# Kernel tuning notes

Measured on AMD Instinct MI355X. Metric: run time of the kernel, lower is better.

Reference implementation:

```python
import jax, jax.numpy as jnp
import numpy as np

GAMMA = 2.0  # args.gamma
B, C, H, W = 8, 21, 512, 512


def setup_inputs() -> dict:
    key = jax.random.key(0)
    k1, k2 = jax.random.split(key)
    pred = jax.random.normal(k1, (B, C, H, W), dtype=jnp.float32)
    # one-hot target built from random per-pixel class labels
    labels = jax.random.randint(k2, (B, H, W), 0, C)
    target = jax.nn.one_hot(labels, C, dtype=jnp.float32)  # [B,H,W,C]
    target = jnp.transpose(target, (0, 3, 1, 2))  # [B,C,H,W]
    return {"pred": pred, "target": target}


def reference(pred, target) -> jnp.ndarray:
    b, c, h, w = pred.shape
    logits = jax.nn.log_softmax(pred, axis=1)  # [B,C,H,W]
    lo = jnp.transpose(logits, (0, 2, 3, 1)).reshape(-1, c)  # [N,C]
    tg = jnp.transpose(target, (0, 2, 3, 1)).reshape(-1, c)  # [N,C]
    n = lo.shape[0]
    beta = (n - 1.0) / n
    # per-pixel focal term summed over channels: sum_j (1-p_j)^gamma * log p_j * t_j
    row_val = jnp.sum((1.0 - jnp.exp(lo)) ** GAMMA * lo * tg, axis=1)  # [N]
    mask = (tg == 1).astype(lo.dtype)  # [N,C] class membership mask
    n_c = jnp.sum(mask, axis=0)  # [C] pixels per class
    class_sum = jnp.einsum('nc,n->c', mask, row_val)  # [C] masked reductions
    w = (1.0 - beta) / (1.0 - jnp.power(jnp.float32(beta), n_c) + 1e-6)  # [C]
    return -jnp.sum(w * class_sum) / n
```

## Files before the change

### kernel.cpp

```cpp
#include <hip/hip_runtime.h>

#define CCH    21
#define HWSZ   (512*512)
#define HW4    (HWSZ/4)
#define NPIX   (8*HWSZ)
#define BLKT   256
#define NBLK   (NPIX/4/BLKT)
#define CB     3
#define NBATCH (CCH/CB)

#define WAIT_VM6() __builtin_amdgcn_s_waitcnt(0x0F70 | 6)
#define WAIT_VM0() __builtin_amdgcn_s_waitcnt(0x0F70 | 0)

typedef float vfloat4 __attribute__((ext_vector_type(4)));

__device__ __forceinline__ void stage16(const float* g, vfloat4* l) {
    __builtin_amdgcn_global_load_lds(
        (const __attribute__((address_space(1))) unsigned int*)g,
        (__attribute__((address_space(3))) unsigned int*)l, 16, 0, 0);
}

__global__ __launch_bounds__(BLKT) void cb_focal_partial(
    const float* __restrict__ pred, const float* __restrict__ targ,
    float* __restrict__ gsum, float* __restrict__ gcnt)
{
    __shared__ vfloat4 sbuf[2][2*CB][BLKT];
    __shared__ float ls_sum[CCH];
    __shared__ float ls_cnt[CCH];
    if (threadIdx.x < CCH) { ls_sum[threadIdx.x] = 0.f; ls_cnt[threadIdx.x] = 0.f; }
    __syncthreads();

    const int tid = blockIdx.x * BLKT + threadIdx.x;
    const int b   = tid >> 16;
    const int hw4 = tid & (HW4 - 1);
    const float* pp = pred + (size_t)b * CCH * HWSZ + (size_t)hw4 * 4;
    const float* tp = targ + (size_t)b * CCH * HWSZ + (size_t)hw4 * 4;
    const int wv = threadIdx.x & 192;

    float s0 = 0.f, s1 = 0.f, s2 = 0.f, s3 = 0.f;
    float vy0 = 0.f, vy1 = 0.f, vy2 = 0.f, vy3 = 0.f;
    float ey0 = 1.f, ey1 = 1.f, ey2 = 1.f, ey3 = 1.f;
    int   y0 = 0, y1 = 0, y2 = 0, y3 = 0;

    auto issue = [&](int k, int buf) {
        #pragma unroll
        for (int j = 0; j < CB; ++j) {
            const size_t coff = (size_t)(k * CB + j) * HWSZ;
            stage16(pp + coff, &sbuf[buf][2*j    ][wv]);
            stage16(tp + coff, &sbuf[buf][2*j + 1][wv]);
        }
    };

    auto compute = [&](int k) {
        #pragma unroll
        for (int j = 0; j < CB; ++j) {
            const vfloat4 v = sbuf[k & 1][2*j    ][threadIdx.x];
            const vfloat4 t = sbuf[k & 1][2*j + 1][threadIdx.x];
            const int c = k * CB + j;
            const float e0 = __expf(v.x), e1 = __expf(v.y),
                        e2 = __expf(v.z), e3 = __expf(v.w);
            s0 += e0; s1 += e1; s2 += e2; s3 += e3;
            const bool h0 = t.x > 0.5f, h1 = t.y > 0.5f,
                       h2 = t.z > 0.5f, h3 = t.w > 0.5f;
            y0 = h0 ? c : y0;  vy0 = h0 ? v.x : vy0;  ey0 = h0 ? e0 : ey0;
            y1 = h1 ? c : y1;  vy1 = h1 ? v.y : vy1;  ey1 = h1 ? e1 : ey1;
            y2 = h2 ? c : y2;  vy2 = h2 ? v.z : vy2;  ey2 = h2 ? e2 : ey2;
            y3 = h3 ? c : y3;  vy3 = h3 ? v.w : vy3;  ey3 = h3 ? e3 : ey3;
        }
    };

    issue(0, 0);
    #pragma unroll
    for (int k = 0; k < NBATCH - 1; ++k) {
        issue(k + 1, (k + 1) & 1);
        __builtin_amdgcn_sched_barrier(0);
        WAIT_VM6();
        __builtin_amdgcn_sched_barrier(0);
        compute(k);
    }
    __builtin_amdgcn_sched_barrier(0);
    WAIT_VM0();
    __builtin_amdgcn_sched_barrier(0);
    compute(NBATCH - 1);

    {
        const float l0 = vy0 - __logf(s0), p0 = ey0 / s0, o0 = 1.f - p0;
        const float l1 = vy1 - __logf(s1), p1 = ey1 / s1, o1 = 1.f - p1;
        const float l2 = vy2 - __logf(s2), p2 = ey2 / s2, o2 = 1.f - p2;
        const float l3 = vy3 - __logf(s3), p3 = ey3 / s3, o3 = 1.f - p3;
        atomicAdd(&ls_sum[y0], o0 * o0 * l0);  atomicAdd(&ls_cnt[y0], 1.f);
        atomicAdd(&ls_sum[y1], o1 * o1 * l1);  atomicAdd(&ls_cnt[y1], 1.f);
        atomicAdd(&ls_sum[y2], o2 * o2 * l2);  atomicAdd(&ls_cnt[y2], 1.f);
        atomicAdd(&ls_sum[y3], o3 * o3 * l3);  atomicAdd(&ls_cnt[y3], 1.f);
    }
    __syncthreads();
    if (threadIdx.x < CCH) {
        atomicAdd(&gsum[threadIdx.x], ls_sum[threadIdx.x]);
        atomicAdd(&gcnt[threadIdx.x], ls_cnt[threadIdx.x]);
    }
}

__global__ void cb_focal_final(const float* __restrict__ gsum,
                               const float* __restrict__ gcnt,
                               float* __restrict__ out)
{
    const int lane = threadIdx.x;
    double term = 0.0;
    if (lane < CCH) {
        const double n    = (double)NPIX;
        const double beta = (n - 1.0) / n;
        const double w = (1.0 - beta) / (1.0 - pow(beta, (double)gcnt[lane]) + 1e-6);
        term = w * (double)gsum[lane];
    }
    for (int off = 32; off; off >>= 1) term += __shfl_down(term, off, 64);
    if (lane == 0) out[0] = (float)(-term / (double)NPIX);
}

extern "C" void kernel_launch(void* const* d_in, const int* in_sizes, int n_in,
                              void* d_out, int out_size, void* d_ws, size_t ws_size,
                              hipStream_t stream) {
    const float* pred = (const float*)d_in[0];
    const float* targ = (const float*)d_in[1];
    float* out  = (float*)d_out;
    float* gsum = (float*)d_ws;
    float* gcnt = gsum + CCH;

    (void)hipMemsetAsync(gsum, 0, 2 * CCH * sizeof(float), stream);
    cb_focal_partial<<<NBLK, BLKT, 0, stream>>>(pred, targ, gsum, gcnt);
    cb_focal_final<<<1, 64, 0, stream>>>(gsum, gcnt, out);
}
```

Measured before the change: 358.4 us.

## Load pred directly into registers, stage only target via LDS in 7-channel batches

Pred values are now read straight into VGPRs with nontemporal vector loads, and only the target tensor is staged through LDS with global_load_lds. Channels are processed in three batches of seven instead of seven batches of three, with double-buffered register and LDS storage. This halves LDS traffic and shared memory use and puts more bytes in flight per wave. In exchange it raises register pressure (two sets of seven vfloat4) and relies on a hand-computed vmcnt wait value being correct.

```diff
diff --git a/kernel.cpp b/kernel.cpp
--- a/kernel.cpp
+++ b/kernel.cpp
@@ -6,11 +6,10 @@
 #define NPIX   (8*HWSZ)
 #define BLKT   256
 #define NBLK   (NPIX/4/BLKT)
-#define CB     3
-#define NBATCH (CCH/CB)
+#define CB     7
+#define NB     3
 
-#define WAIT_VM6() __builtin_amdgcn_s_waitcnt(0x0F70 | 6)
-#define WAIT_VM0() __builtin_amdgcn_s_waitcnt(0x0F70 | 0)
+#define WAIT_VM(n) __builtin_amdgcn_s_waitcnt(0x0F70 | (n))
 
 typedef float vfloat4 __attribute__((ext_vector_type(4)));
 
@@ -24,7 +23,7 @@
     const float* __restrict__ pred, const float* __restrict__ targ,
     float* __restrict__ gsum, float* __restrict__ gcnt)
 {
-    __shared__ vfloat4 sbuf[2][2*CB][BLKT];
+    __shared__ vfloat4 tbuf[2][CB][BLKT];
     __shared__ float ls_sum[CCH];
     __shared__ float ls_cnt[CCH];
     if (threadIdx.x < CCH) { ls_sum[threadIdx.x] = 0.f; ls_cnt[threadIdx.x] = 0.f; }
@@ -42,46 +41,51 @@
     float ey0 = 1.f, ey1 = 1.f, ey2 = 1.f, ey3 = 1.f;
     int   y0 = 0, y1 = 0, y2 = 0, y3 = 0;
 
-    auto issue = [&](int k, int buf) {
+    vfloat4 v[2][CB];
+
+    #pragma unroll
+    for (int j = 0; j < CB; ++j)
+        stage16(tp + (size_t)j * HWSZ, &tbuf[0][j][wv]);
+    #pragma unroll
+    for (int j = 0; j < CB; ++j)
+        v[0][j] = __builtin_nontemporal_load((const vfloat4*)(pp + (size_t)j * HWSZ));
+    __builtin_amdgcn_sched_barrier(0);
+
+    #pragma unroll
+    for (int kk = 0; kk < NB; ++kk) {
+        if (kk + 1 < NB) {
+            #pragma unroll
+            for (int j = 0; j < CB; ++j)
+                stage16(tp + (size_t)((kk + 1) * CB + j) * HWSZ,
+                        &tbuf[(kk + 1) & 1][j][wv]);
+            #pragma unroll
+            for (int j = 0; j < CB; ++j)
+                v[(kk + 1) & 1][j] = __builtin_nontemporal_load(
+                    (const vfloat4*)(pp + (size_t)((kk + 1) * CB + j) * HWSZ));
+            __builtin_amdgcn_sched_barrier(0);
+            WAIT_VM(14);
+        } else {
+            __builtin_amdgcn_sched_barrier(0);
+            WAIT_VM(0);
+        }
+        __builtin_amdgcn_sched_barrier(0);
+
         #pragma unroll
         for (int j = 0; j < CB; ++j) {
-            const size_t coff = (size_t)(k * CB + j) * HWSZ;
-            stage16(pp + coff, &sbuf[buf][2*j    ][wv]);
-            stage16(tp + coff, &sbuf[buf][2*j + 1][wv]);
-        }
-    };
-
-    auto compute = [&](int k) {
-        #pragma unroll
-        for (int j = 0; j < CB; ++j) {
-            const vfloat4 v = sbuf[k & 1][2*j    ][threadIdx.x];
-            const vfloat4 t = sbuf[k & 1][2*j + 1][threadIdx.x];
-            const int c = k * CB + j;
-            const float e0 = __expf(v.x), e1 = __expf(v.y),
-                        e2 = __expf(v.z), e3 = __expf(v.w);
+            const vfloat4 pv = v[kk & 1][j];
+            const vfloat4 t  = tbuf[kk & 1][j][threadIdx.x];
+            const int c = kk * CB + j;
+            const float e0 = __expf(pv.x), e1 = __expf(pv.y),
+                        e2 = __expf(pv.z), e3 = __expf(pv.w);
             s0 += e0; s1 += e1; s2 += e2; s3 += e3;
             const bool h0 = t.x > 0.5f, h1 = t.y > 0.5f,
                        h2 = t.z > 0.5f, h3 = t.w > 0.5f;
-            y0 = h0 ? c : y0;  vy0 = h0 ? v.x : vy0;  ey0 = h0 ? e0 : ey0;
-            y1 = h1 ? c : y1;  vy1 = h1 ? v.y : vy1;  ey1 = h1 ? e1 : ey1;
-            y2 = h2 ? c : y2;  vy2 = h2 ? v.z : vy2;  ey2 = h2 ? e2 : ey2;
-            y3 = h3 ? c : y3;  vy3 = h3 ? v.w : vy3;  ey3 = h3 ? e3 : ey3;
+            y0 = h0 ? c : y0;  vy0 = h0 ? pv.x : vy0;  ey0 = h0 ? e0 : ey0;
+            y1 = h1 ? c : y1;  vy1 = h1 ? pv.y : vy1;  ey1 = h1 ? e1 : ey1;
+            y2 = h2 ? c : y2;  vy2 = h2 ? pv.z : vy2;  ey2 = h2 ? e2 : ey2;
+            y3 = h3 ? c : y3;  vy3 = h3 ? pv.w : vy3;  ey3 = h3 ? e3 : ey3;
         }
-    };
-
-    issue(0, 0);
-    #pragma unroll
-    for (int k = 0; k < NBATCH - 1; ++k) {
-        issue(k + 1, (k + 1) & 1);
-        __builtin_amdgcn_sched_barrier(0);
-        WAIT_VM6();
-        __builtin_amdgcn_sched_barrier(0);
-        compute(k);
     }
-    __builtin_amdgcn_sched_barrier(0);
-    WAIT_VM0();
-    __builtin_amdgcn_sched_barrier(0);
-    compute(NBATCH - 1);
 
     {
         const float l0 = vy0 - __logf(s0), p0 = ey0 / s0, o0 = 1.f - p0;
```

Result: faster. 345.7 us (-3.5%).
